# Kernel tuning notes

Measured on AMD Instinct MI355X. Metric: run time of the kernel, lower is better.

Reference implementation:

```python
import jax, jax.numpy as jnp
import numpy as np

D_MODEL = 512; N_LAYERS = 3; D_INNER = 1024; DT_RANK = 32; D_STATE = 16; D_CONV = 4; RMS_EPS = 1e-5
B, L = 2, 1024


def setup_inputs() -> dict:
    key = jax.random.key(0)
    ks = jax.random.split(key, 8)
    rn = lambda k, s, sc=0.02: jax.random.normal(k, s, jnp.float32) * sc
    # dt bias initialized so softplus(dt_proj_b) falls in [dt_min, dt_max]
    dt = jnp.exp(jax.random.uniform(ks[5], (N_LAYERS, D_INNER)) * (jnp.log(0.1) - jnp.log(0.001)) + jnp.log(0.001))
    return {
        "x": jax.random.normal(ks[0], (B, L, D_MODEL), jnp.float32),
        "in_proj_w": rn(ks[1], (N_LAYERS, 2 * D_INNER, D_MODEL)),
        "conv_w": rn(ks[2], (N_LAYERS, D_INNER, 1, D_CONV), 0.2),
        "conv_b": jnp.zeros((N_LAYERS, D_INNER), jnp.float32),
        "x_proj_w": rn(ks[3], (N_LAYERS, DT_RANK + 2 * D_STATE, D_INNER)),
        "dt_proj_w": rn(ks[4], (N_LAYERS, D_INNER, DT_RANK), 0.1),
        "dt_proj_b": jnp.log(jnp.expm1(dt)),
        "A_log": jnp.log(jnp.broadcast_to(jnp.arange(1, D_STATE + 1, dtype=jnp.float32), (N_LAYERS, D_INNER, D_STATE))),
        "D_skip": jnp.ones((N_LAYERS, D_INNER), jnp.float32),
        "out_proj_w": rn(ks[6], (N_LAYERS, D_MODEL, D_INNER)),
        "norm_w": jnp.ones((N_LAYERS, D_MODEL), jnp.float32),
    }


def _rmsnorm(x, w):
    return x * jax.lax.rsqrt(jnp.mean(x * x, axis=-1, keepdims=True) + RMS_EPS) * w


def _selective_scan(deltaA, deltaBx, C):
    # deltaA, deltaBx: (B, L, ED, N); C: (B, L, N) -> y: (B, L, ED)
    def step(h, inp):
        dA, dBx, c = inp
        h = dA * h + dBx                        # (B, ED, N)
        y = jnp.einsum('ben,bn->be', h, c)      # (B, ED)
        return h, y
    h0 = jnp.zeros((deltaA.shape[0], deltaA.shape[2], deltaA.shape[3]), deltaA.dtype)
    _, ys = jax.lax.scan(step, h0, (jnp.swapaxes(deltaA, 0, 1), jnp.swapaxes(deltaBx, 0, 1), jnp.swapaxes(C, 0, 1)))
    return jnp.swapaxes(ys, 0, 1)


def _mamba_block(u, ipw, cw, cb, xpw, dtw, dtb, A_log, Dp, opw):
    xz = jnp.einsum('bld,ed->ble', u, ipw)      # (B, L, 2*ED)
    x, z = jnp.split(xz, 2, axis=-1)
    xc = jnp.swapaxes(x, 1, 2)                  # (B, ED, L)
    # depthwise causal conv1d (torch pads d_conv-1 both sides then keeps [:L] == left-pad only)
    xc = jax.lax.conv_general_dilated(xc, cw, (1,), [(D_CONV - 1, 0)], feature_group_count=D_INNER) + cb[None, :, None]
    x = jax.nn.silu(jnp.swapaxes(xc, 1, 2))     # (B, L, ED)
    dbc = jnp.einsum('ble,fe->blf', x, xpw)     # (B, L, dt_rank + 2*N)
    delta = dbc[..., :DT_RANK]
    Bm = dbc[..., DT_RANK:DT_RANK + D_STATE]
    Cm = dbc[..., DT_RANK + D_STATE:]
    delta = jax.nn.softplus(jnp.einsum('blr,er->ble', delta, dtw) + dtb)  # (B, L, ED)
    A = -jnp.exp(A_log)                          # (ED, N)
    deltaA = jnp.exp(delta[..., None] * A)       # (B, L, ED, N)
    deltaBx = (delta * x)[..., None] * Bm[:, :, None, :]
    y = _selective_scan(deltaA, deltaBx, Cm) + Dp * x
    y = y * jax.nn.silu(z)
    return jnp.einsum('ble,de->bld', y, opw)


def reference(x, in_proj_w, conv_w, conv_b, x_proj_w, dt_proj_w, dt_proj_b, A_log, D_skip, out_proj_w, norm_w):
    for l in range(N_LAYERS):
        x = x + _mamba_block(_rmsnorm(x, norm_w[l]), in_proj_w[l], conv_w[l], conv_b[l], x_proj_w[l],
                             dt_proj_w[l], dt_proj_b[l], A_log[l], D_skip[l], out_proj_w[l])
    return x
```

## Files before the change

kernel.cpp:

```cpp
#include <hip/hip_runtime.h>
#include <hip/hip_bf16.h>
#include <math.h>

#define D_MODEL   512
#define N_LAYERS  3
#define D_INNER   1024
#define DT_RANK   32
#define D_STATE   16
#define D_CONV    4
#define RMS_EPS   1e-5f
#define B_SZ      2
#define L_SEQ     1024
#define NTOK      (B_SZ * L_SEQ)
#define NC        64
#define CT        16

typedef __bf16 bf16_t;
typedef bf16_t bf16x8 __attribute__((ext_vector_type(8)));
typedef float  f32x4  __attribute__((ext_vector_type(4)));

#define CVT_N1 (N_LAYERS * 2 * D_INNER * D_MODEL)
#define CVT_N2 (N_LAYERS * 64 * D_INNER)
#define CVT_N3 (N_LAYERS * D_INNER * DT_RANK)
#define CVT_N4 (N_LAYERS * D_MODEL * D_INNER)
#define CVT_S1 (CVT_N1 / 8)
#define CVT_S2 (CVT_S1 + CVT_N2 / 8)
#define CVT_S3 (CVT_S2 + CVT_N3 / 8)
#define CVT_S4 (CVT_S3 + CVT_N4 / 8)
#define CVT_S5 (CVT_S4 + NTOK * D_MODEL / 4)
#define CVT_BLOCKS ((CVT_S5 + 255) / 256)

__device__ __forceinline__ void cvt8(const float* s, bf16_t* d, int idx) {
    int i = idx * 8;
    f32x4 v0 = *(const f32x4*)&s[i];
    f32x4 v1 = *(const f32x4*)&s[i + 4];
    bf16x8 o;
#pragma unroll
    for (int j = 0; j < 4; j++) { o[j] = (bf16_t)v0[j]; o[j + 4] = (bf16_t)v1[j]; }
    *(bf16x8*)&d[i] = o;
}

__global__ __launch_bounds__(256) void cvt_all(const float* __restrict__ ipw,
                                               const float* __restrict__ xpw,
                                               const float* __restrict__ dtw,
                                               const float* __restrict__ opw,
                                               const float* __restrict__ x,
                                               bf16_t* __restrict__ wip,
                                               bf16_t* __restrict__ wxp,
                                               bf16_t* __restrict__ wdt,
                                               bf16_t* __restrict__ wop,
                                               float* __restrict__ out) {
    int t = blockIdx.x * 256 + threadIdx.x;
    if (t < CVT_S1)      cvt8(ipw, wip, t);
    else if (t < CVT_S2) cvt8(xpw, wxp, t - CVT_S1);
    else if (t < CVT_S3) cvt8(dtw, wdt, t - CVT_S2);
    else if (t < CVT_S4) cvt8(opw, wop, t - CVT_S3);
    else if (t < CVT_S5) {
        int i = (t - CVT_S4) * 4;
        *(f32x4*)&out[i] = *(const f32x4*)&x[i];
    }
}

__global__ __launch_bounds__(256) void rms_scale(const float* __restrict__ x,
                                                 float* __restrict__ scales,
                                                 float* __restrict__ dbcf) {
    dbcf[blockIdx.x * 256 + threadIdx.x] = 0.f;
    int wid  = threadIdx.x >> 6;
    int lane = threadIdx.x & 63;
    int token = blockIdx.x * 4 + wid;
    const float* xr = x + (size_t)token * D_MODEL;
    f32x4 v0 = *(const f32x4*)&xr[lane * 8];
    f32x4 v1 = *(const f32x4*)&xr[lane * 8 + 4];
    float ss = 0.f;
#pragma unroll
    for (int i = 0; i < 4; i++) ss += v0[i] * v0[i] + v1[i] * v1[i];
#pragma unroll
    for (int m = 32; m >= 1; m >>= 1) ss += __shfl_xor(ss, m, 64);
    if (lane == 0) scales[token] = rsqrtf(ss * (1.0f / D_MODEL) + RMS_EPS);
}

__global__ __launch_bounds__(256) void inproj_gemm(const float* __restrict__ x,
                                                   const float* __restrict__ scales,
                                                   const float* __restrict__ nw,
                                                   const bf16_t* __restrict__ W,
                                                   bf16_t* __restrict__ xz) {
    __shared__ bf16_t As[128][72];
    __shared__ bf16_t Bs[128][72];
    int tid = threadIdx.x;
    int m0 = blockIdx.y * 128, n0 = blockIdx.x * 128;
    int wid = tid >> 6, lane = tid & 63;
    int wm = (wid >> 1) * 64, wn = (wid & 1) * 64;
    int lr = lane & 15, kg = lane >> 4;

    f32x4 acc[4][4] = {};

    int srow = tid >> 1, scol = (tid & 1) * 32;
    float rs = scales[m0 + srow];
    const float*  xp = x + (size_t)(m0 + srow) * D_MODEL + scol;
    const bf16_t* wp = W + (size_t)(n0 + srow) * D_MODEL + scol;

    for (int k0 = 0; k0 < D_MODEL; k0 += 64) {
#pragma unroll
        for (int g = 0; g < 4; g++) {
            f32x4 v0 = *(const f32x4*)(xp + k0 + g * 8);
            f32x4 v1 = *(const f32x4*)(xp + k0 + g * 8 + 4);
            f32x4 g0 = *(const f32x4*)(nw + k0 + scol + g * 8);
            f32x4 g1 = *(const f32x4*)(nw + k0 + scol + g * 8 + 4);
            bf16x8 a;
#pragma unroll
            for (int j = 0; j < 4; j++) {
                a[j]     = (bf16_t)(v0[j] * rs * g0[j]);
                a[j + 4] = (bf16_t)(v1[j] * rs * g1[j]);
            }
            *(bf16x8*)&As[srow][scol + g * 8] = a;
            *(bf16x8*)&Bs[srow][scol + g * 8] = *(const bf16x8*)(wp + k0 + g * 8);
        }
        __syncthreads();
#pragma unroll
        for (int kk = 0; kk < 2; kk++) {
            bf16x8 af[4], bfr[4];
#pragma unroll
            for (int f = 0; f < 4; f++) {
                af[f]  = *(const bf16x8*)&As[wm + f * 16 + lr][kk * 32 + kg * 8];
                bfr[f] = *(const bf16x8*)&Bs[wn + f * 16 + lr][kk * 32 + kg * 8];
            }
#pragma unroll
            for (int fm = 0; fm < 4; fm++)
#pragma unroll
                for (int fn = 0; fn < 4; fn++)
                    acc[fm][fn] = __builtin_amdgcn_mfma_f32_16x16x32_bf16(af[fm], bfr[fn], acc[fm][fn], 0, 0, 0);
        }
        __syncthreads();
    }

    int colb = lane & 15, rowb = (lane >> 4) * 4;
#pragma unroll
    for (int fm = 0; fm < 4; fm++)
#pragma unroll
        for (int fn = 0; fn < 4; fn++)
#pragma unroll
            for (int r = 0; r < 4; r++) {
                int row = m0 + wm + fm * 16 + rowb + r;
                int col = n0 + wn + fn * 16 + colb;
                xz[(size_t)row * (2 * D_INNER) + col] = (bf16_t)acc[fm][fn][r];
            }
}

__global__ __launch_bounds__(256) void xproj_conv(const bf16_t* __restrict__ xz,
                                                  const float* __restrict__ cw,
                                                  const float* __restrict__ cb,
                                                  const bf16_t* __restrict__ Wx,
                                                  bf16_t* __restrict__ xc,
                                                  float* __restrict__ dbcf) {
    __shared__ bf16_t As[64][40];
    __shared__ bf16_t Bs[64][40];
    int tid = threadIdx.x;
    int kc = blockIdx.x;
    int m0 = blockIdx.y * 64;
    int wid = tid >> 6, lane = tid & 63;
    int wm = (wid >> 1) * 32, wn = (wid & 1) * 32;
    int lr = lane & 15, kg = lane >> 4;

    f32x4 acc[2][2] = {};
    int srow = tid >> 2, scol = (tid & 3) * 8;
    int token = m0 + srow;
    int l = token & (L_SEQ - 1);
    const bf16_t* base = xz + (size_t)token * (2 * D_INNER) + kc * 128 + scol;
    const bf16_t* b1 = base - (l >= 1 ? 1 : 0) * 2 * D_INNER;
    const bf16_t* b2 = base - (l >= 2 ? 2 : 0) * 2 * D_INNER;
    const bf16_t* b3 = base - (l >= 3 ? 3 : 0) * 2 * D_INNER;
    const bf16_t* wrow = Wx + (size_t)srow * D_INNER + kc * 128 + scol;

    for (int k0 = 0; k0 < 128; k0 += 32) {
        int e = kc * 128 + k0 + scol;
        bf16x8 t0v = *(const bf16x8*)(base + k0);
        bf16x8 t1v = *(const bf16x8*)(b1 + k0);
        bf16x8 t2v = *(const bf16x8*)(b2 + k0);
        bf16x8 t3v = *(const bf16x8*)(b3 + k0);
        bf16x8 a;
#pragma unroll
        for (int j = 0; j < 8; j++) {
            f32x4 w = *(const f32x4*)&cw[(e + j) * 4];
            float av = cb[e + j] + w[3] * (float)t0v[j];
            if (l >= 1) av += w[2] * (float)t1v[j];
            if (l >= 2) av += w[1] * (float)t2v[j];
            if (l >= 3) av += w[0] * (float)t3v[j];
            a[j] = (bf16_t)(av / (1.f + __expf(-av)));
        }
        *(bf16x8*)&As[srow][scol] = a;
        *(bf16x8*)&xc[(size_t)token * D_INNER + e] = a;
        *(bf16x8*)&Bs[srow][scol] = *(const bf16x8*)(wrow + k0);
        __syncthreads();
        bf16x8 a0 = *(const bf16x8*)&As[wm + lr][kg * 8];
        bf16x8 a1 = *(const bf16x8*)&As[wm + 16 + lr][kg * 8];
        bf16x8 b0 = *(const bf16x8*)&Bs[wn + lr][kg * 8];
        bf16x8 bb1 = *(const bf16x8*)&Bs[wn + 16 + lr][kg * 8];
        acc[0][0] = __builtin_amdgcn_mfma_f32_16x16x32_bf16(a0, b0, acc[0][0], 0, 0, 0);
        acc[0][1] = __builtin_amdgcn_mfma_f32_16x16x32_bf16(a0, bb1, acc[0][1], 0, 0, 0);
        acc[1][0] = __builtin_amdgcn_mfma_f32_16x16x32_bf16(a1, b0, acc[1][0], 0, 0, 0);
        acc[1][1] = __builtin_amdgcn_mfma_f32_16x16x32_bf16(a1, bb1, acc[1][1], 0, 0, 0);
        __syncthreads();
    }

    int colb = lane & 15, rowb = (lane >> 4) * 4;
#pragma unroll
    for (int fm = 0; fm < 2; fm++)
#pragma unroll
        for (int fn = 0; fn < 2; fn++)
#pragma unroll
            for (int r = 0; r < 4; r++) {
                int row = m0 + wm + fm * 16 + rowb + r;
                int col = wn + fn * 16 + colb;
                atomicAdd(&dbcf[(size_t)row * 64 + col], acc[fm][fn][r]);
            }
}

__global__ __launch_bounds__(256) void dtscan1(const float* __restrict__ dbcf,
                                               const bf16_t* __restrict__ Wd,
                                               const float* __restrict__ dtb,
                                               const bf16_t* __restrict__ xc,
                                               const float* __restrict__ A_log,
                                               float* __restrict__ delta,
                                               float* __restrict__ cs) {
    __shared__ bf16_t As[64][40];
    __shared__ bf16_t Bw[64][40];
    __shared__ float  ds_[64][65];
    __shared__ float  Bsc[64][17];
    int tid = threadIdx.x;
    int n0 = blockIdx.x * 64, m0 = blockIdx.y * 64;
    int wid = tid >> 6, lane = tid & 63;
    int wm = (wid >> 1) * 32, wn = (wid & 1) * 32;
    int lr = lane & 15, kg = lane >> 4;

    int srow = tid >> 2, scol = (tid & 3) * 8;
    f32x4 v0 = *(const f32x4*)&dbcf[(size_t)(m0 + srow) * 64 + scol];
    f32x4 v1 = *(const f32x4*)&dbcf[(size_t)(m0 + srow) * 64 + scol + 4];
    bf16x8 a;
#pragma unroll
    for (int j = 0; j < 4; j++) { a[j] = (bf16_t)v0[j]; a[j + 4] = (bf16_t)v1[j]; }
    *(bf16x8*)&As[srow][scol] = a;
    *(bf16x8*)&Bw[srow][scol] = *(const bf16x8*)(Wd + (size_t)(n0 + srow) * DT_RANK + scol);
    __syncthreads();

    bf16x8 a0 = *(const bf16x8*)&As[wm + lr][kg * 8];
    bf16x8 a1 = *(const bf16x8*)&As[wm + 16 + lr][kg * 8];
    bf16x8 b0 = *(const bf16x8*)&Bw[wn + lr][kg * 8];
    bf16x8 b1 = *(const bf16x8*)&Bw[wn + 16 + lr][kg * 8];
    f32x4 acc[2][2] = {};
    acc[0][0] = __builtin_amdgcn_mfma_f32_16x16x32_bf16(a0, b0, acc[0][0], 0, 0, 0);
    acc[0][1] = __builtin_amdgcn_mfma_f32_16x16x32_bf16(a0, b1, acc[0][1], 0, 0, 0);
    acc[1][0] = __builtin_amdgcn_mfma_f32_16x16x32_bf16(a1, b0, acc[1][0], 0, 0, 0);
    acc[1][1] = __builtin_amdgcn_mfma_f32_16x16x32_bf16(a1, b1, acc[1][1], 0, 0, 0);

    int colb = lane & 15, rowb = (lane >> 4) * 4;
#pragma unroll
    for (int fm = 0; fm < 2; fm++)
#pragma unroll
        for (int fn = 0; fn < 2; fn++)
#pragma unroll
            for (int r = 0; r < 4; r++) {
                int row = wm + fm * 16 + rowb + r;
                int el  = wn + fn * 16 + colb;
                float t = acc[fm][fn][r] + dtb[n0 + el];
                float sp = (t > 15.f) ? t : log1pf(__expf(t));
                delta[(size_t)(m0 + row) * D_INNER + (n0 + el)] = sp;
                ds_[row][el] = sp;
            }
    for (int i = tid; i < 64 * 16; i += 256)
        Bsc[i >> 4][i & 15] = dbcf[(size_t)(m0 + (i >> 4)) * 64 + 32 + (i & 15)];
    __syncthreads();

    int cl = tid >> 6, el = tid & 63;
    int e  = n0 + el;
    int b  = m0 >> 10;
    int chunk = ((m0 & (L_SEQ - 1)) >> 4) + cl;

    float Aa[16], h[16], P[16];
    const float* Ae = A_log + (size_t)e * D_STATE;
#pragma unroll
    for (int n = 0; n < 16; n++) { Aa[n] = -__expf(Ae[n]); h[n] = 0.f; P[n] = 1.f; }

    const bf16_t* xp = xc + (size_t)(m0 + cl * CT) * D_INNER + e;
    float xvs[CT];
#pragma unroll
    for (int j = 0; j < CT; j++) xvs[j] = (float)xp[j * D_INNER];

#pragma unroll
    for (int l = 0; l < CT; ++l) {
        float dv = ds_[cl * CT + l][el];
        float dx = dv * xvs[l];
#pragma unroll
        for (int n = 0; n < 16; n++) {
            float dA = __expf(dv * Aa[n]);
            h[n] = dA * h[n] + dx * Bsc[cl * CT + l][n];
            P[n] *= dA;
        }
    }

    float* o = cs + (size_t)(b * NC + chunk) * 32 * D_INNER + e;
#pragma unroll
    for (int n = 0; n < 16; n++) {
        o[n * D_INNER]        = P[n];
        o[(16 + n) * D_INNER] = h[n];
    }
}

__global__ __launch_bounds__(256) void scan_combine(float* __restrict__ cs) {
    int e = blockIdx.x * 256 + threadIdx.x;
    int n = blockIdx.y;
    int b = blockIdx.z;
    size_t stride = (size_t)32 * D_INNER;
    float* p = cs + ((size_t)b * NC * 32 + n) * D_INNER + e;

    float h = 0.f;
    for (int base = 0; base < NC; base += 8) {
        float Pv[8], hv[8];
#pragma unroll
        for (int j = 0; j < 8; j++) {
            Pv[j] = p[(base + j) * stride];
            hv[j] = p[(base + j) * stride + 16 * D_INNER];
        }
#pragma unroll
        for (int j = 0; j < 8; j++) {
            p[(base + j) * stride] = h;
            h = Pv[j] * h + hv[j];
        }
    }
}

__global__ __launch_bounds__(256) void scan_part3(const float* __restrict__ delta,
                                                  const bf16_t* __restrict__ xc,
                                                  const float* __restrict__ dbcf,
                                                  const bf16_t* __restrict__ xz,
                                                  const float* __restrict__ A_log,
                                                  const float* __restrict__ Dskip,
                                                  const float* __restrict__ cs,
                                                  bf16_t* __restrict__ yz) {
    int e = blockIdx.x * 256 + threadIdx.x;
    int c = blockIdx.y;
    int b = blockIdx.z;
    size_t t0 = (size_t)b * L_SEQ + (size_t)c * CT;

    __shared__ float BCs[CT][32];
    for (int i = threadIdx.x; i < CT * 32; i += 256)
        BCs[i >> 5][i & 31] = dbcf[(t0 + (i >> 5)) * 64 + 32 + (i & 31)];
    __syncthreads();

    float Aa[16], h[16];
    const float* Ae = A_log + (size_t)e * D_STATE;
    const float* hi = cs + (size_t)(b * NC + c) * 32 * D_INNER + e;
#pragma unroll
    for (int n = 0; n < 16; n++) {
        Aa[n] = -__expf(Ae[n]);
        h[n]  = hi[n * D_INNER];
    }
    float Dv = Dskip[e];

    const float*  dp = delta + t0 * D_INNER + e;
    const bf16_t* xp = xc    + t0 * D_INNER + e;
    const bf16_t* zp = xz    + t0 * 2 * D_INNER + D_INNER + e;
    bf16_t*       yp = yz    + t0 * D_INNER + e;

    float dvs[CT], xvs[CT], zvs[CT];
#pragma unroll
    for (int j = 0; j < CT; j++) dvs[j] = dp[j * D_INNER];
#pragma unroll
    for (int j = 0; j < CT; j++) xvs[j] = (float)xp[j * D_INNER];
#pragma unroll
    for (int j = 0; j < CT; j++) zvs[j] = (float)zp[j * 2 * D_INNER];

#pragma unroll
    for (int l = 0; l < CT; ++l) {
        float dx = dvs[l] * xvs[l];
        float y  = Dv * xvs[l];
#pragma unroll
        for (int n = 0; n < 16; n++) {
            float dA = __expf(dvs[l] * Aa[n]);
            h[n] = dA * h[n] + dx * BCs[l][n];
            y   += h[n] * BCs[l][16 + n];
        }
        float zv = zvs[l];
        yp[l * D_INNER] = (bf16_t)(y * (zv / (1.f + __expf(-zv))));
    }
}

__global__ __launch_bounds__(256) void outproj_gemm(const bf16_t* __restrict__ A,
                                                    const bf16_t* __restrict__ W,
                                                    float* __restrict__ out) {
    __shared__ bf16_t As[64][72];
    __shared__ bf16_t Bs[64][72];
    int tid = threadIdx.x;
    int m0 = blockIdx.y * 64, n0 = blockIdx.x * 64;
    int wid = tid >> 6, lane = tid & 63;
    int wm = (wid >> 1) * 32, wn = (wid & 1) * 32;
    int lr = lane & 15, kg = lane >> 4;

    f32x4 acc[2][2] = {};
    int srow = tid >> 2, scol = (tid & 3) * 16;
    const bf16_t* Ap = A + (size_t)(m0 + srow) * D_INNER + scol;
    const bf16_t* Wp = W + (size_t)(n0 + srow) * D_INNER + scol;

    for (int k0 = 0; k0 < D_INNER; k0 += 64) {
        *(bf16x8*)&As[srow][scol]     = *(const bf16x8*)(Ap + k0);
        *(bf16x8*)&As[srow][scol + 8] = *(const bf16x8*)(Ap + k0 + 8);
        *(bf16x8*)&Bs[srow][scol]     = *(const bf16x8*)(Wp + k0);
        *(bf16x8*)&Bs[srow][scol + 8] = *(const bf16x8*)(Wp + k0 + 8);
        __syncthreads();
#pragma unroll
        for (int kk = 0; kk < 2; kk++) {
            bf16x8 a0 = *(const bf16x8*)&As[wm + lr][kk * 32 + kg * 8];
            bf16x8 a1 = *(const bf16x8*)&As[wm + 16 + lr][kk * 32 + kg * 8];
            bf16x8 b0 = *(const bf16x8*)&Bs[wn + lr][kk * 32 + kg * 8];
            bf16x8 b1 = *(const bf16x8*)&Bs[wn + 16 + lr][kk * 32 + kg * 8];
            acc[0][0] = __builtin_amdgcn_mfma_f32_16x16x32_bf16(a0, b0, acc[0][0], 0, 0, 0);
            acc[0][1] = __builtin_amdgcn_mfma_f32_16x16x32_bf16(a0, b1, acc[0][1], 0, 0, 0);
            acc[1][0] = __builtin_amdgcn_mfma_f32_16x16x32_bf16(a1, b0, acc[1][0], 0, 0, 0);
            acc[1][1] = __builtin_amdgcn_mfma_f32_16x16x32_bf16(a1, b1, acc[1][1], 0, 0, 0);
        }
        __syncthreads();
    }

    int colb = lane & 15, rowb = (lane >> 4) * 4;
#pragma unroll
    for (int fm = 0; fm < 2; fm++)
#pragma unroll
        for (int fn = 0; fn < 2; fn++)
#pragma unroll
            for (int r = 0; r < 4; r++) {
                int row = m0 + wm + fm * 16 + rowb + r;
                int col = n0 + wn + fn * 16 + colb;
                out[(size_t)row * D_MODEL + col] += acc[fm][fn][r];
            }
}

extern "C" void kernel_launch(void* const* d_in, const int* in_sizes, int n_in,
                              void* d_out, int out_size, void* d_ws, size_t ws_size,
                              hipStream_t stream) {
    const float* x_in  = (const float*)d_in[0];
    const float* ipw   = (const float*)d_in[1];
    const float* cw    = (const float*)d_in[2];
    const float* cb    = (const float*)d_in[3];
    const float* xpw   = (const float*)d_in[4];
    const float* dtw   = (const float*)d_in[5];
    const float* dtb   = (const float*)d_in[6];
    const float* A_log = (const float*)d_in[7];
    const float* Dsk   = (const float*)d_in[8];
    const float* opw   = (const float*)d_in[9];
    const float* nw    = (const float*)d_in[10];
    float* out = (float*)d_out;

    char* ws = (char*)d_ws;
    size_t off = 0;
    auto alloc = [&](size_t bytes) -> void* {
        void* p = ws + off;
        off += (bytes + 255) & ~(size_t)255;
        return p;
    };
    bf16_t* wip    = (bf16_t*)alloc((size_t)CVT_N1 * 2);
    bf16_t* wxp    = (bf16_t*)alloc((size_t)CVT_N2 * 2);
    bf16_t* wdt    = (bf16_t*)alloc((size_t)CVT_N3 * 2);
    bf16_t* wop    = (bf16_t*)alloc((size_t)CVT_N4 * 2);
    bf16_t* xz_bf  = (bf16_t*)alloc((size_t)NTOK * 2 * D_INNER * 2);
    bf16_t* xc_bf  = (bf16_t*)alloc((size_t)NTOK * D_INNER * 2);
    float*  dbcf   = (float*)alloc((size_t)NTOK * 64 * 4);
    float*  deltaf = (float*)alloc((size_t)NTOK * D_INNER * 4);
    bf16_t* yz_bf  = (bf16_t*)alloc((size_t)NTOK * D_INNER * 2);
    float*  scales = (float*)alloc((size_t)NTOK * 4);
    float*  cstate = (float*)alloc((size_t)B_SZ * NC * 32 * D_INNER * 4);

    cvt_all<<<CVT_BLOCKS, 256, 0, stream>>>(ipw, xpw, dtw, opw, x_in,
                                            wip, wxp, wdt, wop, out);

    for (int l = 0; l < N_LAYERS; ++l) {
        const float* Al = A_log + (size_t)l * D_INNER * D_STATE;
        rms_scale<<<NTOK / 4, 256, 0, stream>>>(out, scales, dbcf);
        inproj_gemm<<<dim3(2 * D_INNER / 128, NTOK / 128), 256, 0, stream>>>(
            out, scales, nw + (size_t)l * D_MODEL,
            wip + (size_t)l * 2 * D_INNER * D_MODEL, xz_bf);
        xproj_conv<<<dim3(8, NTOK / 64), 256, 0, stream>>>(
            xz_bf, cw + (size_t)l * D_INNER * D_CONV, cb + (size_t)l * D_INNER,
            wxp + (size_t)l * 64 * D_INNER, xc_bf, dbcf);
        dtscan1<<<dim3(D_INNER / 64, NTOK / 64), 256, 0, stream>>>(
            dbcf, wdt + (size_t)l * D_INNER * DT_RANK, dtb + (size_t)l * D_INNER,
            xc_bf, Al, deltaf, cstate);
        scan_combine<<<dim3(D_INNER / 256, D_STATE, B_SZ), 256, 0, stream>>>(cstate);
        scan_part3<<<dim3(D_INNER / 256, NC, B_SZ), 256, 0, stream>>>(
            deltaf, xc_bf, dbcf, xz_bf, Al, Dsk + (size_t)l * D_INNER, cstate, yz_bf);
        outproj_gemm<<<dim3(D_MODEL / 64, NTOK / 64), 256, 0, stream>>>(
            yz_bf, wop + (size_t)l * D_MODEL * D_INNER, out);
    }
}
```

Measured before the change: 278.4 us.

## Fuse RMSNorm sum-of-squares into previous kernels and shrink in-proj GEMM tile

Removes the per-layer rms_scale kernel. Each token's sum of squares is now accumulated with atomics in the epilogue of the previous out-projection GEMM, or in the initial copy kernel for the first layer. The zeroing of sumsq and dbcf moves into scan_part3 and outproj_gemm, and the in-projection GEMM computes the rsqrt itself. The in-proj GEMM tile also shrinks from 128x128 to 128x64, doubling the block count for better occupancy. The trade-off is atomic contention and a tighter web of ordering dependencies between kernels.

Result: slower. 316.9 us (+13.8%).

```diff
diff --git a/kernel.cpp b/kernel.cpp
--- a/kernel.cpp
+++ b/kernel.cpp
@@ -18,6 +18,7 @@
 typedef __bf16 bf16_t;
 typedef bf16_t bf16x8 __attribute__((ext_vector_type(8)));
 typedef float  f32x4  __attribute__((ext_vector_type(4)));
+typedef float  f32x2  __attribute__((ext_vector_type(2)));
 
 #define CVT_N1 (N_LAYERS * 2 * D_INNER * D_MODEL)
 #define CVT_N2 (N_LAYERS * 64 * D_INNER)
@@ -28,7 +29,8 @@
 #define CVT_S3 (CVT_S2 + CVT_N3 / 8)
 #define CVT_S4 (CVT_S3 + CVT_N4 / 8)
 #define CVT_S5 (CVT_S4 + NTOK * D_MODEL / 4)
-#define CVT_BLOCKS ((CVT_S5 + 255) / 256)
+#define CVT_S6 (CVT_S5 + NTOK * 64 / 4)
+#define CVT_BLOCKS ((CVT_S6 + 255) / 256)
 
 __device__ __forceinline__ void cvt8(const float* s, bf16_t* d, int idx) {
     int i = idx * 8;
@@ -49,7 +51,9 @@
                                                bf16_t* __restrict__ wxp,
                                                bf16_t* __restrict__ wdt,
                                                bf16_t* __restrict__ wop,
-                                               float* __restrict__ out) {
+                                               float* __restrict__ out,
+                                               float* __restrict__ sumsq,
+                                               float* __restrict__ dbcf) {
     int t = blockIdx.x * 256 + threadIdx.x;
     if (t < CVT_S1)      cvt8(ipw, wip, t);
     else if (t < CVT_S2) cvt8(xpw, wxp, t - CVT_S1);
@@ -57,47 +61,39 @@
     else if (t < CVT_S4) cvt8(opw, wop, t - CVT_S3);
     else if (t < CVT_S5) {
         int i = (t - CVT_S4) * 4;
-        *(f32x4*)&out[i] = *(const f32x4*)&x[i];
-    }
-}
-
-__global__ __launch_bounds__(256) void rms_scale(const float* __restrict__ x,
-                                                 float* __restrict__ scales,
-                                                 float* __restrict__ dbcf) {
-    dbcf[blockIdx.x * 256 + threadIdx.x] = 0.f;
-    int wid  = threadIdx.x >> 6;
-    int lane = threadIdx.x & 63;
-    int token = blockIdx.x * 4 + wid;
-    const float* xr = x + (size_t)token * D_MODEL;
-    f32x4 v0 = *(const f32x4*)&xr[lane * 8];
-    f32x4 v1 = *(const f32x4*)&xr[lane * 8 + 4];
-    float ss = 0.f;
-#pragma unroll
-    for (int i = 0; i < 4; i++) ss += v0[i] * v0[i] + v1[i] * v1[i];
-#pragma unroll
-    for (int m = 32; m >= 1; m >>= 1) ss += __shfl_xor(ss, m, 64);
-    if (lane == 0) scales[token] = rsqrtf(ss * (1.0f / D_MODEL) + RMS_EPS);
+        f32x4 v = *(const f32x4*)&x[i];
+        *(f32x4*)&out[i] = v;
+        float s = v[0]*v[0] + v[1]*v[1] + v[2]*v[2] + v[3]*v[3];
+#pragma unroll
+        for (int m = 32; m >= 1; m >>= 1) s += __shfl_xor(s, m, 64);
+        if ((threadIdx.x & 63) == 0) atomicAdd(&sumsq[i >> 9], s);
+    } else if (t < CVT_S6) {
+        int i = (t - CVT_S5) * 4;
+        f32x4 z = {0.f, 0.f, 0.f, 0.f};
+        *(f32x4*)&dbcf[i] = z;
+    }
 }
 
 __global__ __launch_bounds__(256) void inproj_gemm(const float* __restrict__ x,
-                                                   const float* __restrict__ scales,
+                                                   const float* __restrict__ sumsq,
                                                    const float* __restrict__ nw,
                                                    const bf16_t* __restrict__ W,
                                                    bf16_t* __restrict__ xz) {
     __shared__ bf16_t As[128][72];
-    __shared__ bf16_t Bs[128][72];
+    __shared__ bf16_t Bs[64][72];
     int tid = threadIdx.x;
-    int m0 = blockIdx.y * 128, n0 = blockIdx.x * 128;
+    int n0 = blockIdx.x * 64, m0 = blockIdx.y * 128;
     int wid = tid >> 6, lane = tid & 63;
-    int wm = (wid >> 1) * 64, wn = (wid & 1) * 64;
+    int wm = (wid >> 1) * 64, wn = (wid & 1) * 32;
     int lr = lane & 15, kg = lane >> 4;
 
-    f32x4 acc[4][4] = {};
+    f32x4 acc[4][2] = {};
 
     int srow = tid >> 1, scol = (tid & 1) * 32;
-    float rs = scales[m0 + srow];
+    int srB  = tid >> 2, scB  = (tid & 3) * 16;
+    float rs = rsqrtf(sumsq[m0 + srow] * (1.0f / D_MODEL) + RMS_EPS);
     const float*  xp = x + (size_t)(m0 + srow) * D_MODEL + scol;
-    const bf16_t* wp = W + (size_t)(n0 + srow) * D_MODEL + scol;
+    const bf16_t* wp = W + (size_t)(n0 + srB) * D_MODEL + scB;
 
     for (int k0 = 0; k0 < D_MODEL; k0 += 64) {
 #pragma unroll
@@ -113,21 +109,23 @@
                 a[j + 4] = (bf16_t)(v1[j] * rs * g1[j]);
             }
             *(bf16x8*)&As[srow][scol + g * 8] = a;
-            *(bf16x8*)&Bs[srow][scol + g * 8] = *(const bf16x8*)(wp + k0 + g * 8);
-        }
+        }
+        *(bf16x8*)&Bs[srB][scB]     = *(const bf16x8*)(wp + k0);
+        *(bf16x8*)&Bs[srB][scB + 8] = *(const bf16x8*)(wp + k0 + 8);
         __syncthreads();
 #pragma unroll
         for (int kk = 0; kk < 2; kk++) {
-            bf16x8 af[4], bfr[4];
-#pragma unroll
-            for (int f = 0; f < 4; f++) {
-                af[f]  = *(const bf16x8*)&As[wm + f * 16 + lr][kk * 32 + kg * 8];
+            bf16x8 af[4], bfr[2];
+#pragma unroll
+            for (int f = 0; f < 4; f++)
+                af[f] = *(const bf16x8*)&As[wm + f * 16 + lr][kk * 32 + kg * 8];
+#pragma unroll
+            for (int f = 0; f < 2; f++)
                 bfr[f] = *(const bf16x8*)&Bs[wn + f * 16 + lr][kk * 32 + kg * 8];
-            }
 #pragma unroll
             for (int fm = 0; fm < 4; fm++)
 #pragma unroll
-                for (int fn = 0; fn < 4; fn++)
+                for (int fn = 0; fn < 2; fn++)
                     acc[fm][fn] = __builtin_amdgcn_mfma_f32_16x16x32_bf16(af[fm], bfr[fn], acc[fm][fn], 0, 0, 0);
         }
         __syncthreads();
@@ -137,7 +135,7 @@
 #pragma unroll
     for (int fm = 0; fm < 4; fm++)
 #pragma unroll
-        for (int fn = 0; fn < 4; fn++)
+        for (int fn = 0; fn < 2; fn++)
 #pragma unroll
             for (int r = 0; r < 4; r++) {
                 int row = m0 + wm + fm * 16 + rowb + r;
@@ -335,10 +333,12 @@
                                                   const float* __restrict__ A_log,
                                                   const float* __restrict__ Dskip,
                                                   const float* __restrict__ cs,
-                                                  bf16_t* __restrict__ yz) {
+                                                  bf16_t* __restrict__ yz,
+                                                  float* __restrict__ sumsq) {
     int e = blockIdx.x * 256 + threadIdx.x;
     int c = blockIdx.y;
     int b = blockIdx.z;
+    if (b == 0 && c < 2) sumsq[c * 1024 + (blockIdx.x & 3) * 256 + threadIdx.x] = 0.f;
     size_t t0 = (size_t)b * L_SEQ + (size_t)c * CT;
 
     __shared__ float BCs[CT][32];
@@ -386,7 +386,9 @@
 
 __global__ __launch_bounds__(256) void outproj_gemm(const bf16_t* __restrict__ A,
                                                     const bf16_t* __restrict__ W,
-                                                    float* __restrict__ out) {
+                                                    float* __restrict__ out,
+                                                    float* __restrict__ sumsq,
+                                                    float* __restrict__ dbcf) {
     __shared__ bf16_t As[64][72];
     __shared__ bf16_t Bs[64][72];
     int tid = threadIdx.x;
@@ -394,6 +396,12 @@
     int wid = tid >> 6, lane = tid & 63;
     int wm = (wid >> 1) * 32, wn = (wid & 1) * 32;
     int lr = lane & 15, kg = lane >> 4;
+
+    {
+        int flat = blockIdx.y * 8 + blockIdx.x;
+        f32x2 z = {0.f, 0.f};
+        *(f32x2*)&dbcf[(size_t)flat * 512 + tid * 2] = z;
+    }
 
     f32x4 acc[2][2] = {};
     int srow = tid >> 2, scol = (tid & 3) * 16;
@@ -421,6 +429,7 @@
     }
 
     int colb = lane & 15, rowb = (lane >> 4) * 4;
+    float rowsq[2][4] = {};
 #pragma unroll
     for (int fm = 0; fm < 2; fm++)
 #pragma unroll
@@ -429,8 +438,23 @@
             for (int r = 0; r < 4; r++) {
                 int row = m0 + wm + fm * 16 + rowb + r;
                 int col = n0 + wn + fn * 16 + colb;
-                out[(size_t)row * D_MODEL + col] += acc[fm][fn][r];
+                size_t idx = (size_t)row * D_MODEL + col;
+                float vn = out[idx] + acc[fm][fn][r];
+                out[idx] = vn;
+                rowsq[fm][r] += vn * vn;
             }
+#pragma unroll
+    for (int fm = 0; fm < 2; fm++)
+#pragma unroll
+        for (int r = 0; r < 4; r++) {
+            float s = rowsq[fm][r];
+            s += __shfl_xor(s, 1, 64);
+            s += __shfl_xor(s, 2, 64);
+            s += __shfl_xor(s, 4, 64);
+            s += __shfl_xor(s, 8, 64);
+            if ((lane & 15) == 0)
+                atomicAdd(&sumsq[m0 + wm + fm * 16 + rowb + r], s);
+        }
 }
 
 extern "C" void kernel_launch(void* const* d_in, const int* in_sizes, int n_in,
@@ -465,17 +489,17 @@
     float*  dbcf   = (float*)alloc((size_t)NTOK * 64 * 4);
     float*  deltaf = (float*)alloc((size_t)NTOK * D_INNER * 4);
     bf16_t* yz_bf  = (bf16_t*)alloc((size_t)NTOK * D_INNER * 2);
-    float*  scales = (float*)alloc((size_t)NTOK * 4);
+    float*  sumsq  = (float*)alloc((size_t)NTOK * 4);
     float*  cstate = (float*)alloc((size_t)B_SZ * NC * 32 * D_INNER * 4);
 
+    hipMemsetAsync(sumsq, 0, NTOK * sizeof(float), stream);
     cvt_all<<<CVT_BLOCKS, 256, 0, stream>>>(ipw, xpw, dtw, opw, x_in,
-                                            wip, wxp, wdt, wop, out);
+                                            wip, wxp, wdt, wop, out, sumsq, dbcf);
 
     for (int l = 0; l < N_LAYERS; ++l) {
         const float* Al = A_log + (size_t)l * D_INNER * D_STATE;
-        rms_scale<<<NTOK / 4, 256, 0, stream>>>(out, scales, dbcf);
-        inproj_gemm<<<dim3(2 * D_INNER / 128, NTOK / 128), 256, 0, stream>>>(
-            out, scales, nw + (size_t)l * D_MODEL,
+        inproj_gemm<<<dim3(2 * D_INNER / 64, NTOK / 128), 256, 0, stream>>>(
+            out, sumsq, nw + (size_t)l * D_MODEL,
             wip + (size_t)l * 2 * D_INNER * D_MODEL, xz_bf);
         xproj_conv<<<dim3(8, NTOK / 64), 256, 0, stream>>>(
             xz_bf, cw + (size_t)l * D_INNER * D_CONV, cb + (size_t)l * D_INNER,
@@ -485,8 +509,9 @@
             xc_bf, Al, deltaf, cstate);
         scan_combine<<<dim3(D_INNER / 256, D_STATE, B_SZ), 256, 0, stream>>>(cstate);
         scan_part3<<<dim3(D_INNER / 256, NC, B_SZ), 256, 0, stream>>>(
-            deltaf, xc_bf, dbcf, xz_bf, Al, Dsk + (size_t)l * D_INNER, cstate, yz_bf);
+            deltaf, xc_bf, dbcf, xz_bf, Al, Dsk + (size_t)l * D_INNER, cstate,
+            yz_bf, sumsq);
         outproj_gemm<<<dim3(D_MODEL / 64, NTOK / 64), 256, 0, stream>>>(
-            yz_bf, wop + (size_t)l * D_MODEL * D_INNER, out);
-    }
-}
+            yz_bf, wop + (size_t)l * D_MODEL * D_INNER, out, sumsq, dbcf);
+    }
+}
```
